# Kernel optimization log

Hardware: AMD Instinct MI355X
Metric: run time of the kernel (lower is better)

The kernel has to match this reference:

```python
import jax, jax.numpy as jnp
import numpy as np

B, L, D, H, DFF, WS = 8, 16384, 256, 8, 1024, 32
HD = D // H
NW = L // WS


def setup_inputs() -> dict:
    key = jax.random.key(0)
    ks = jax.random.split(key, 12)
    p = lambda k, sh: jax.random.normal(k, sh, jnp.float32) * 0.02
    return {
        "query_em": jax.random.normal(ks[0], (B, L, D), jnp.float32),
        "key_value_em": jax.random.normal(ks[1], (B, L, D), jnp.float32),
        "Wq": p(ks[2], (D, D)), "bq": jnp.zeros((D,), jnp.float32),
        "Wk": p(ks[3], (D, D)), "bk": jnp.zeros((D,), jnp.float32),
        "Wv": p(ks[4], (D, D)), "bv": jnp.zeros((D,), jnp.float32),
        "Wo": p(ks[5], (D, D)), "bo": jnp.zeros((D,), jnp.float32),
        "g1": jnp.ones((D,), jnp.float32), "be1": jnp.zeros((D,), jnp.float32),
        "W1": p(ks[6], (D, DFF)), "bf1": jnp.zeros((DFF,), jnp.float32),
        "W2": p(ks[7], (DFF, D)), "bf2": jnp.zeros((D,), jnp.float32),
        "g2": jnp.ones((D,), jnp.float32), "be2": jnp.zeros((D,), jnp.float32),
    }


def _layernorm(x, g, b):
    m = jnp.mean(x, axis=-1, keepdims=True)
    v = jnp.var(x, axis=-1, keepdims=True)
    return (x - m) * jax.lax.rsqrt(v + 1e-5) * g + b


def _encoder_layer(q, kv, Wq, bq, Wk, bk, Wv, bv, Wo, bo, g1, be1, W1, bf1, W2, bf2, g2, be2):
    # q, kv: [B, NW, WS, D] -- attention only within each window of WS tokens
    b, nw, ws, d = q.shape
    qh = (q @ Wq + bq).reshape(b, nw, ws, H, HD)
    kh = (kv @ Wk + bk).reshape(b, nw, ws, H, HD)
    vh = (kv @ Wv + bv).reshape(b, nw, ws, H, HD)
    scores = jnp.einsum("bnqhd,bnkhd->bnhqk", qh, kh) / np.sqrt(HD).astype(np.float32)
    attn = jax.nn.softmax(scores, axis=-1)
    o = jnp.einsum("bnhqk,bnkhd->bnqhd", attn, vh).reshape(b, nw, ws, d)
    o = o @ Wo + bo
    x = _layernorm(q + o, g1, be1)  # post-LN residual
    f = jax.nn.relu(x @ W1 + bf1) @ W2 + bf2
    return _layernorm(x + f, g2, be2)


def reference(query_em, key_value_em, Wq, bq, Wk, bk, Wv, bv, Wo, bo,
              g1, be1, W1, bf1, W2, bf2, g2, be2):
    params = (Wq, bq, Wk, bk, Wv, bv, Wo, bo, g1, be1, W1, bf1, W2, bf2, g2, be2)
    q = query_em.reshape(B, NW, WS, D)
    kv = key_value_em.reshape(B, NW, WS, D)
    x = _encoder_layer(q, kv, *params)
    # cyclic shift by half a window-count along the window axis, second pass, shift back
    x = jnp.roll(x, -WS // 2, axis=1)
    x = _encoder_layer(x, x, *params)
    x = jnp.roll(x, WS // 2, axis=1)
    return x.reshape(B, L, D)
```

## Files before the change

kernel.cpp:

```cpp
#include <hip/hip_runtime.h>
#include <cstdint>
#include <cstddef>

typedef unsigned short u16;
typedef __bf16 bf16x8 __attribute__((ext_vector_type(8)));
typedef float f32x4 __attribute__((ext_vector_type(4)));
typedef unsigned short u16x8 __attribute__((ext_vector_type(8)));
typedef unsigned short u16x4 __attribute__((ext_vector_type(4)));

__device__ __forceinline__ u16 f2bf(float f) {
  union { float f; unsigned u; } x; x.f = f;
  unsigned r = x.u + 0x7fffu + ((x.u >> 16) & 1u);
  return (u16)(r >> 16);
}
__device__ __forceinline__ float bf2f(u16 u) {
  union { unsigned u; float f; } x; x.u = ((unsigned)u) << 16;
  return x.f;
}
__device__ __forceinline__ void gload16(const void* g, void* l) {
  __builtin_amdgcn_global_load_lds(
      (const __attribute__((address_space(1))) unsigned int*)g,
      (__attribute__((address_space(3))) unsigned int*)l, 16, 0, 0);
}

template<int MODE>
__global__ __launch_bounds__(256) void gemm_bt(
    const u16* __restrict__ Ap, int lda, const u16* __restrict__ Bt,
    const float* __restrict__ bias, u16* __restrict__ C0, int ldc, int coff,
    u16* __restrict__ C2, int vsplit, int N, int K, int gy)
{
  __shared__ u16 As[2][128 * 32];
  __shared__ u16 Bs[2][128 * 32];
  const int tid  = threadIdx.x;
  const int lane = tid & 63, w = tid >> 6;
  const int nwg = gridDim.x, o = blockIdx.x;
  const int lid = (o & 7) * (nwg >> 3) + (o >> 3);
  const int by = lid % gy, bx = lid / gy;
  const int row0 = bx * 128, col0 = by * 128;
  const int wr = (w >> 1) * 64, wc = (w & 1) * 64;
  const int fr = lane & 15, fg = lane >> 4;
  const int srow  = (w << 5) + (lane >> 2);
  const int sslot = (lane & 3) ^ ((lane >> 2) & 3);

  auto stage = [&](int buf, int k0) {
    #pragma unroll
    for (int h = 0; h < 2; ++h)
      gload16((const char*)Ap + ((size_t)(row0 + srow + h*16) * lda + k0) * 2 + sslot*16,
              &As[buf][((w << 5) + h*16) * 32]);
    #pragma unroll
    for (int h = 0; h < 2; ++h)
      gload16((const char*)Bt + ((size_t)(col0 + srow + h*16) * K + k0) * 2 + sslot*16,
              &Bs[buf][((w << 5) + h*16) * 32]);
  };

  f32x4 acc[4][4] = {};

  stage(0, 0);
  __syncthreads();
  int cur = 0;
  for (int k0 = 0; k0 < K; k0 += 32) {
    if (k0 + 32 < K) stage(cur ^ 1, k0 + 32);
    bf16x8 af[4], bf[4];
    #pragma unroll
    for (int i = 0; i < 4; ++i) {
      const int r = wr + i*16 + fr;
      af[i] = *(const bf16x8*)&As[cur][r*32 + ((fg ^ (fr & 3)) << 3)];
    }
    #pragma unroll
    for (int j = 0; j < 4; ++j) {
      const int r = wc + j*16 + fr;
      bf[j] = *(const bf16x8*)&Bs[cur][r*32 + ((fg ^ (fr & 3)) << 3)];
    }
    #pragma unroll
    for (int i = 0; i < 4; ++i)
      #pragma unroll
      for (int j = 0; j < 4; ++j)
        acc[i][j] = __builtin_amdgcn_mfma_f32_16x16x32_bf16(af[i], bf[j], acc[i][j], 0, 0, 0);
    __syncthreads();
    cur ^= 1;
  }

  const int vpart = (MODE == 3) || (MODE == 2 && col0 >= vsplit);
  #pragma unroll
  for (int j = 0; j < 4; ++j) {
    const int c  = col0 + wc + j*16 + fr;
    const float bv = bias[c];
    #pragma unroll
    for (int i = 0; i < 4; ++i) {
      if (vpart) {
        const int cv = (MODE == 2) ? c - vsplit : c;
        const int rb = row0 + wr + i*16 + fg*4;
        u16x4 vv;
        #pragma unroll
        for (int t = 0; t < 4; ++t) vv[t] = f2bf(acc[i][j][t] + bv);
        *(u16x4*)&C2[((size_t)(rb >> 5) * 256 + cv) * 32 + (rb & 31)] = vv;
      } else {
        #pragma unroll
        for (int t = 0; t < 4; ++t) {
          const int r = row0 + wr + i*16 + fg*4 + t;
          float v = acc[i][j][t] + bv;
          if (MODE == 1) v = v > 0.f ? v : 0.f;
          C0[(size_t)r * ldc + coff + c] = f2bf(v);
        }
      }
    }
  }
}

template<int OUT_F32>
__global__ __launch_bounds__(512, 2) void ffn_fused(
    const u16* __restrict__ X, const u16* __restrict__ W1T,
    const float* __restrict__ b1, const u16* __restrict__ W2T,
    const float* __restrict__ b2, const float* __restrict__ g,
    const float* __restrict__ be, void* __restrict__ Y)
{
  __shared__ u16 W1s[4][32 * 256];
  __shared__ u16 W2s[4][256 * 32];
  __shared__ u16 Hs[8][32 * 32];
  __shared__ float b1s[1024];
  const int tid = threadIdx.x, lane = tid & 63, w = tid >> 6;
  const int fr = lane & 15, fg = lane >> 4;
  const int row0 = blockIdx.x * 256 + w * 32;
  u16* Hw = &Hs[w][0];
  const int hxor = (fr >> 1) & 3;

  auto stage = [&](int buf, int hb) {
    #pragma unroll
    for (int h = 0; h < 2; ++h) {
      const int r = w*4 + h*2 + (lane >> 5);
      const int sl = (lane & 31) ^ (r & 7);
      gload16((const char*)W1T + ((size_t)((hb << 5) + r) * 256 + sl*8) * 2,
              &W1s[buf][(w*4 + h*2) * 256]);
    }
    #pragma unroll
    for (int h = 0; h < 2; ++h) {
      const int r = w*32 + h*16 + (lane >> 2);
      const int sl = (lane & 3) ^ ((r >> 1) & 3);
      gload16((const char*)W2T + ((size_t)r * 1024 + (hb << 5) + sl*8) * 2,
              &W2s[buf][(w*32 + h*16) * 32]);
    }
  };

  if (tid < 256) {
    f32x4 bv = *(const f32x4*)&b1[tid * 4];
    *(f32x4*)&b1s[tid * 4] = bv;
  }
  bf16x8 af[2][8];
  #pragma unroll
  for (int g2 = 0; g2 < 2; ++g2)
    #pragma unroll
    for (int kf = 0; kf < 8; ++kf)
      af[g2][kf] = *(const bf16x8*)&X[(size_t)(row0 + g2*16 + fr) * 256 + kf*32 + fg*8];
  asm volatile("s_waitcnt vmcnt(0)" ::: "memory");

  f32x4 acc2[2][16] = {};

  auto compute_slice = [&](int hb, int cur) {
    f32x4 acc1[2][2] = {};
    #pragma unroll
    for (int kf = 0; kf < 8; ++kf) {
      #pragma unroll
      for (int hf = 0; hf < 2; ++hf) {
        const int n = hf*16 + fr;
        bf16x8 w1f = *(const bf16x8*)&W1s[cur][n*256 + ((((kf << 2) | fg) ^ (n & 7)) << 3)];
        acc1[hf][0] = __builtin_amdgcn_mfma_f32_16x16x32_bf16(w1f, af[0][kf], acc1[hf][0], 0, 0, 0);
        acc1[hf][1] = __builtin_amdgcn_mfma_f32_16x16x32_bf16(w1f, af[1][kf], acc1[hf][1], 0, 0, 0);
      }
    }
    #pragma unroll
    for (int g2 = 0; g2 < 2; ++g2) {
      #pragma unroll
      for (int hf = 0; hf < 2; ++hf) {
        const int h0 = hf*16 + fg*4;
        f32x4 b4 = *(const f32x4*)&b1s[(hb << 5) + h0];
        u16x4 hv;
        #pragma unroll
        for (int t = 0; t < 4; ++t) {
          float v = acc1[hf][g2][t] + b4[t];
          hv[t] = f2bf(v > 0.f ? v : 0.f);
        }
        const int tok = g2*16 + fr;
        *(u16x4*)((char*)Hw + tok*64 + ((((hf << 1) | (fg >> 1)) ^ hxor) << 4)
                                     + ((fg & 1) << 3)) = hv;
      }
    }
    asm volatile("s_waitcnt lgkmcnt(0)" ::: "memory");
    __builtin_amdgcn_sched_barrier(0);

    bf16x8 hf2[2];
    #pragma unroll
    for (int g2 = 0; g2 < 2; ++g2) {
      const int tok = g2*16 + fr;
      hf2[g2] = *(const bf16x8*)((char*)Hw + tok*64 + ((fg ^ hxor) << 4));
    }
    #pragma unroll
    for (int nf = 0; nf < 16; ++nf) {
      const int n = nf*16 + fr;
      bf16x8 w2f = *(const bf16x8*)&W2s[cur][n*32 + ((fg ^ ((n >> 1) & 3)) << 3)];
      acc2[0][nf] = __builtin_amdgcn_mfma_f32_16x16x32_bf16(hf2[0], w2f, acc2[0][nf], 0, 0, 0);
      acc2[1][nf] = __builtin_amdgcn_mfma_f32_16x16x32_bf16(hf2[1], w2f, acc2[1][nf], 0, 0, 0);
    }
  };

  stage(0, 0);
  stage(1, 1);
  for (int hb = 0; hb < 30; ++hb) {
    stage((hb + 2) & 3, hb + 2);
    asm volatile("s_waitcnt vmcnt(8)" ::: "memory");
    __builtin_amdgcn_s_barrier();
    __builtin_amdgcn_sched_barrier(0);
    compute_slice(hb, hb & 3);
  }
  asm volatile("s_waitcnt vmcnt(4)" ::: "memory");
  __builtin_amdgcn_s_barrier();
  __builtin_amdgcn_sched_barrier(0);
  compute_slice(30, 30 & 3);
  asm volatile("s_waitcnt vmcnt(0)" ::: "memory");
  __builtin_amdgcn_s_barrier();
  __builtin_amdgcn_sched_barrier(0);
  compute_slice(31, 31 & 3);

  #pragma unroll
  for (int g2 = 0; g2 < 2; ++g2) {
    const int rbase = row0 + g2*16 + fg*4;
    float s1[4] = {}, sq[4] = {};
    #pragma unroll
    for (int nf = 0; nf < 16; ++nf) {
      const int c = nf*16 + fr;
      const float b = b2[c];
      #pragma unroll
      for (int t = 0; t < 4; ++t) {
        float v = acc2[g2][nf][t] + b + bf2f(X[(size_t)(rbase + t) * 256 + c]);
        acc2[g2][nf][t] = v;
        s1[t] += v; sq[t] += v * v;
      }
    }
    #pragma unroll
    for (int d = 1; d < 16; d <<= 1) {
      #pragma unroll
      for (int t = 0; t < 4; ++t) {
        s1[t] += __shfl_xor(s1[t], d, 64);
        sq[t] += __shfl_xor(sq[t], d, 64);
      }
    }
    float mean[4], rstd[4];
    #pragma unroll
    for (int t = 0; t < 4; ++t) {
      mean[t] = s1[t] * (1.f/256.f);
      const float var = sq[t] * (1.f/256.f) - mean[t]*mean[t];
      rstd[t] = rsqrtf(var + 1e-5f);
    }
    #pragma unroll
    for (int nf = 0; nf < 16; ++nf) {
      const int c = nf*16 + fr;
      const float gc = g[c], bc = be[c];
      #pragma unroll
      for (int t = 0; t < 4; ++t) {
        const float y = (acc2[g2][nf][t] - mean[t]) * rstd[t] * gc + bc;
        if (OUT_F32) ((float*)Y)[(size_t)(rbase + t) * 256 + c] = y;
        else         ((u16*)Y)[(size_t)(rbase + t) * 256 + c] = f2bf(y);
      }
    }
  }
}

__global__ __launch_bounds__(256) void attn_mfma(
    const u16* Q, int sq, const u16* __restrict__ K, int sk,
    const u16* __restrict__ Vt, u16* O, int so)
{
  __shared__ u16 P[4][32 * 40];
  const int tid = threadIdx.x, lane = tid & 63, w = tid >> 6;
  const int win = blockIdx.x * 4 + w;
  const size_t q0 = (size_t)win * 32;
  const int fr = lane & 15, fg = lane >> 4;
  u16* Pw = &P[w][0];
  const float scale = 0.17677669529663687f;

  for (int h = 0; h < 8; ++h) {
    const int co = h * 32;
    bf16x8 qa[2], kb[2];
    #pragma unroll
    for (int i = 0; i < 2; ++i)
      qa[i] = *(const bf16x8*)&Q[(q0 + i*16 + fr) * sq + co + fg*8];
    #pragma unroll
    for (int j = 0; j < 2; ++j)
      kb[j] = *(const bf16x8*)&K[(q0 + j*16 + fr) * sk + co + fg*8];
    f32x4 s[2][2] = {};
    #pragma unroll
    for (int i = 0; i < 2; ++i)
      #pragma unroll
      for (int j = 0; j < 2; ++j)
        s[i][j] = __builtin_amdgcn_mfma_f32_16x16x32_bf16(qa[i], kb[j], s[i][j], 0, 0, 0);

    float inv[2][4];
    #pragma unroll
    for (int i = 0; i < 2; ++i) {
      #pragma unroll
      for (int t = 0; t < 4; ++t) {
        float a0 = s[i][0][t] * scale, a1 = s[i][1][t] * scale;
        float mx = fmaxf(a0, a1);
        #pragma unroll
        for (int d = 1; d < 16; d <<= 1) mx = fmaxf(mx, __shfl_xor(mx, d, 64));
        const float p0 = __expf(a0 - mx), p1 = __expf(a1 - mx);
        float sm = p0 + p1;
        #pragma unroll
        for (int d = 1; d < 16; d <<= 1) sm += __shfl_xor(sm, d, 64);
        inv[i][t] = 1.f / sm;
        const int q = i*16 + fg*4 + t;
        Pw[q*40 + fr]      = f2bf(p0);
        Pw[q*40 + 16 + fr] = f2bf(p1);
      }
    }

    bf16x8 pa[2], vb[2];
    #pragma unroll
    for (int i = 0; i < 2; ++i)
      pa[i] = *(const bf16x8*)&Pw[(i*16 + fr)*40 + fg*8];
    #pragma unroll
    for (int j = 0; j < 2; ++j)
      vb[j] = *(const bf16x8*)&Vt[(size_t)win*8192 + (co + j*16 + fr)*32 + fg*8];
    f32x4 oacc[2][2] = {};
    #pragma unroll
    for (int i = 0; i < 2; ++i)
      #pragma unroll
      for (int j = 0; j < 2; ++j)
        oacc[i][j] = __builtin_amdgcn_mfma_f32_16x16x32_bf16(pa[i], vb[j], oacc[i][j], 0, 0, 0);

    #pragma unroll
    for (int i = 0; i < 2; ++i)
      #pragma unroll
      for (int j = 0; j < 2; ++j)
        #pragma unroll
        for (int t = 0; t < 4; ++t)
          O[(q0 + i*16 + fg*4 + t) * so + co + j*16 + fr] =
              f2bf(oacc[i][j][t] * inv[i][t]);
  }
}

__global__ __launch_bounds__(256) void ln_resid(
    const u16* __restrict__ X, const u16* __restrict__ R,
    const float* __restrict__ g, const float* __restrict__ be,
    u16* __restrict__ Y)
{
  const int tid = threadIdx.x;
  const int lane = tid & 63, w = tid >> 6;
  const size_t row = (size_t)blockIdx.x * 4 + w;
  const size_t off = row * 256 + (size_t)(lane << 2);
  u16x4 xb = *(const u16x4*)&X[off];
  u16x4 rb = *(const u16x4*)&R[off];
  const float v0 = bf2f(xb[0]) + bf2f(rb[0]), v1 = bf2f(xb[1]) + bf2f(rb[1]);
  const float v2 = bf2f(xb[2]) + bf2f(rb[2]), v3 = bf2f(xb[3]) + bf2f(rb[3]);
  float s  = v0 + v1 + v2 + v3;
  float s2 = v0*v0 + v1*v1 + v2*v2 + v3*v3;
  #pragma unroll
  for (int d = 1; d < 64; d <<= 1) {
    s  += __shfl_xor(s,  d, 64);
    s2 += __shfl_xor(s2, d, 64);
  }
  const float m   = s  * (1.f/256.f);
  const float var = s2 * (1.f/256.f) - m*m;
  const float rs  = rsqrtf(var + 1e-5f);
  f32x4 gg = *(const f32x4*)&g[lane << 2];
  f32x4 bb = *(const f32x4*)&be[lane << 2];
  u16x4 oo = { f2bf((v0 - m) * rs * gg[0] + bb[0]),
               f2bf((v1 - m) * rs * gg[1] + bb[1]),
               f2bf((v2 - m) * rs * gg[2] + bb[2]),
               f2bf((v3 - m) * rs * gg[3] + bb[3]) };
  *(u16x4*)&Y[off] = oo;
}

__global__ __launch_bounds__(256) void wprep(
    const float* __restrict__ W, u16* __restrict__ Wt, int K, int N)
{
  const int idx = blockIdx.x * 256 + threadIdx.x;
  if (idx >= K * N) return;
  const int k = idx / N, n = idx - k * N;
  Wt[(size_t)n * K + k] = f2bf(W[idx]);
}

__global__ __launch_bounds__(256) void bcat(
    const float* __restrict__ a, const float* __restrict__ b,
    const float* __restrict__ c, float* __restrict__ o)
{
  const int i = blockIdx.x * 256 + threadIdx.x;
  o[i] = i < 256 ? a[i] : (i < 512 ? b[i - 256] : c[i - 512]);
}

__global__ __launch_bounds__(256) void f32_to_bf16(
    const float* __restrict__ X, u16* __restrict__ Y)
{
  const size_t i = ((size_t)blockIdx.x * 256 + threadIdx.x) * 8;
  f32x4 a = *(const f32x4*)&X[i];
  f32x4 b = *(const f32x4*)&X[i + 4];
  u16x8 o = { f2bf(a[0]), f2bf(a[1]), f2bf(a[2]), f2bf(a[3]),
              f2bf(b[0]), f2bf(b[1]), f2bf(b[2]), f2bf(b[3]) };
  *(u16x8*)&Y[i] = o;
}

extern "C" void kernel_launch(void* const* d_in, const int* in_sizes, int n_in,
                              void* d_out, int out_size, void* d_ws, size_t ws_size,
                              hipStream_t stream)
{
  const float* query  = (const float*)d_in[0];
  const float* keyval = (const float*)d_in[1];
  const float* Wq = (const float*)d_in[2];  const float* bq  = (const float*)d_in[3];
  const float* Wk = (const float*)d_in[4];  const float* bk  = (const float*)d_in[5];
  const float* Wv = (const float*)d_in[6];  const float* bv  = (const float*)d_in[7];
  const float* Wo = (const float*)d_in[8];  const float* bo  = (const float*)d_in[9];
  const float* g1 = (const float*)d_in[10]; const float* be1 = (const float*)d_in[11];
  const float* W1 = (const float*)d_in[12]; const float* bf1 = (const float*)d_in[13];
  const float* W2 = (const float*)d_in[14]; const float* bf2 = (const float*)d_in[15];
  const float* g2 = (const float*)d_in[16]; const float* be2 = (const float*)d_in[17];

  const int M = 131072;
  char* ws = (char*)d_ws;
  u16*  xcur = (u16*)ws;
  u16*  x1   = (u16*)(ws + (64ull  << 20));
  u16*  kvb  = (u16*)(ws + (128ull << 20));
  u16*  tmp  = (u16*)(ws + (192ull << 20));
  u16*  QKc  = (u16*)(ws + (256ull << 20));
  u16*  Vtc  = (u16*)(ws + (384ull << 20));
  u16*  WqkvT = (u16*)(ws + (448ull << 20));
  u16*  WoT   = WqkvT + 196608;
  u16*  W1T   = WoT   + 65536;
  u16*  W2T   = W1T   + 262144;
  float* bqkv = (float*)(W2T + 262144);
  float* bkv  = bqkv + 256;

  wprep<<<256,  256, 0, stream>>>(Wq, WqkvT,          256, 256);
  wprep<<<256,  256, 0, stream>>>(Wk, WqkvT +  65536, 256, 256);
  wprep<<<256,  256, 0, stream>>>(Wv, WqkvT + 131072, 256, 256);
  wprep<<<256,  256, 0, stream>>>(Wo, WoT, 256, 256);
  wprep<<<1024, 256, 0, stream>>>(W1, W1T, 256, 1024);
  wprep<<<1024, 256, 0, stream>>>(W2, W2T, 1024, 256);
  bcat<<<3, 256, 0, stream>>>(bq, bk, bv, bqkv);
  f32_to_bf16<<<16384, 256, 0, stream>>>(query,  xcur);
  f32_to_bf16<<<16384, 256, 0, stream>>>(keyval, kvb);

  auto run_layer = [&](int first, int last) {
    if (first) {
      gemm_bt<0><<<2048, 256, 0, stream>>>(
          xcur, 256, WqkvT, bq, QKc, 512, 0, nullptr, 0, 256, 256, 2);
      gemm_bt<2><<<4096, 256, 0, stream>>>(
          kvb, 256, WqkvT + 65536, bkv, QKc, 512, 256, Vtc, 256, 512, 256, 4);
    } else {
      gemm_bt<2><<<6144, 256, 0, stream>>>(
          xcur, 256, WqkvT, bqkv, QKc, 512, 0, Vtc, 512, 768, 256, 6);
    }
    attn_mfma<<<1024, 256, 0, stream>>>(QKc, 512, QKc + 256, 512, Vtc, QKc, 512);
    gemm_bt<0><<<2048, 256, 0, stream>>>(
        QKc, 512, WoT, bo, tmp, 256, 0, nullptr, 0, 256, 256, 2);
    ln_resid<<<M/4, 256, 0, stream>>>(tmp, xcur, g1, be1, x1);
    if (last) ffn_fused<1><<<512, 512, 0, stream>>>(
        x1, W1T, bf1, W2T, bf2, g2, be2, d_out);
    else      ffn_fused<0><<<512, 512, 0, stream>>>(
        x1, W1T, bf1, W2T, bf2, g2, be2, xcur);
  };

  run_layer(1, 0);
  run_layer(0, 1);
}
```

Baseline: 938.1 us.

## Fuse output projection GEMM with residual add and LayerNorm

Replaces the separate Wo GEMM and ln_resid kernels with one kernel. Each block computes full 128x256 output rows, adds bias and residual, reduces row statistics through shuffles and shared memory, and writes the normalized bf16 result. This removes the round trip of the intermediate tensor through global memory and one kernel launch per layer. In exchange it uses a new tiling with 512 threads and more LDS, and its epilogue does scalar strided residual loads and stores.

```diff
diff --git a/kernel.cpp b/kernel.cpp
--- a/kernel.cpp
+++ b/kernel.cpp
@@ -107,6 +107,122 @@
   }
 }
 
+__global__ __launch_bounds__(512) void gemm_oln(
+    const u16* __restrict__ Ap, int lda, const u16* __restrict__ Bt,
+    const float* __restrict__ bias, const u16* __restrict__ Res,
+    const float* __restrict__ g, const float* __restrict__ be,
+    u16* __restrict__ Y, int K)
+{
+  __shared__ u16 As[2][128 * 32];
+  __shared__ u16 Bs[2][256 * 32];
+  __shared__ float2 red[128][4];
+  __shared__ float2 stats[128];
+  const int tid  = threadIdx.x;
+  const int lane = tid & 63, w = tid >> 6;
+  const int nwg = gridDim.x, o = blockIdx.x;
+  const int lid = (o & 7) * (nwg >> 3) + (o >> 3);
+  const int row0 = lid * 128;
+  const int wr = (w >> 2) * 64, wc = (w & 3) * 64;
+  const int fr = lane & 15, fg = lane >> 4;
+  const int sr   = lane >> 2;
+  const int sslot = (lane & 3) ^ ((lane >> 2) & 3);
+
+  auto stage = [&](int buf, int k0) {
+    gload16((const char*)Ap + ((size_t)(row0 + (w << 4) + sr) * lda + k0) * 2 + sslot*16,
+            &As[buf][((w << 4)) * 32]);
+    #pragma unroll
+    for (int h = 0; h < 2; ++h)
+      gload16((const char*)Bt + ((size_t)((w << 5) + h*16 + sr) * K + k0) * 2 + sslot*16,
+              &Bs[buf][((w << 5) + h*16) * 32]);
+  };
+
+  f32x4 acc[4][4] = {};
+
+  stage(0, 0);
+  __syncthreads();
+  int cur = 0;
+  for (int k0 = 0; k0 < K; k0 += 32) {
+    if (k0 + 32 < K) stage(cur ^ 1, k0 + 32);
+    bf16x8 af[4], bf[4];
+    #pragma unroll
+    for (int i = 0; i < 4; ++i) {
+      const int r = wr + i*16 + fr;
+      af[i] = *(const bf16x8*)&As[cur][r*32 + ((fg ^ (fr & 3)) << 3)];
+    }
+    #pragma unroll
+    for (int j = 0; j < 4; ++j) {
+      const int r = wc + j*16 + fr;
+      bf[j] = *(const bf16x8*)&Bs[cur][r*32 + ((fg ^ (fr & 3)) << 3)];
+    }
+    #pragma unroll
+    for (int i = 0; i < 4; ++i)
+      #pragma unroll
+      for (int j = 0; j < 4; ++j)
+        acc[i][j] = __builtin_amdgcn_mfma_f32_16x16x32_bf16(af[i], bf[j], acc[i][j], 0, 0, 0);
+    __syncthreads();
+    cur ^= 1;
+  }
+
+  float ps[4][4] = {}, pq[4][4] = {};
+  #pragma unroll
+  for (int j = 0; j < 4; ++j) {
+    const int c = wc + j*16 + fr;
+    const float bv = bias[c];
+    #pragma unroll
+    for (int i = 0; i < 4; ++i) {
+      #pragma unroll
+      for (int t = 0; t < 4; ++t) {
+        const int r = row0 + wr + i*16 + fg*4 + t;
+        float v = acc[i][j][t] + bv + bf2f(Res[(size_t)r * 256 + c]);
+        acc[i][j][t] = v;
+        ps[i][t] += v;
+        pq[i][t] += v * v;
+      }
+    }
+  }
+  #pragma unroll
+  for (int d = 1; d < 16; d <<= 1) {
+    #pragma unroll
+    for (int i = 0; i < 4; ++i)
+      #pragma unroll
+      for (int t = 0; t < 4; ++t) {
+        ps[i][t] += __shfl_xor(ps[i][t], d, 64);
+        pq[i][t] += __shfl_xor(pq[i][t], d, 64);
+      }
+  }
+  if (fr == 0) {
+    #pragma unroll
+    for (int i = 0; i < 4; ++i)
+      #pragma unroll
+      for (int t = 0; t < 4; ++t)
+        red[wr + i*16 + fg*4 + t][w & 3] = make_float2(ps[i][t], pq[i][t]);
+  }
+  __syncthreads();
+  if (tid < 128) {
+    float S = 0.f, Q = 0.f;
+    #pragma unroll
+    for (int ww = 0; ww < 4; ++ww) { float2 p = red[tid][ww]; S += p.x; Q += p.y; }
+    const float m = S * (1.f/256.f);
+    const float var = Q * (1.f/256.f) - m*m;
+    stats[tid] = make_float2(m, rsqrtf(var + 1e-5f));
+  }
+  __syncthreads();
+  #pragma unroll
+  for (int i = 0; i < 4; ++i) {
+    #pragma unroll
+    for (int t = 0; t < 4; ++t) {
+      const int rl = wr + i*16 + fg*4 + t;
+      const float2 st = stats[rl];
+      const size_t r = row0 + rl;
+      #pragma unroll
+      for (int j = 0; j < 4; ++j) {
+        const int c = wc + j*16 + fr;
+        Y[r * 256 + c] = f2bf((acc[i][j][t] - st.x) * st.y * g[c] + be[c]);
+      }
+    }
+  }
+}
+
 template<int OUT_F32>
 __global__ __launch_bounds__(512, 2) void ffn_fused(
     const u16* __restrict__ X, const u16* __restrict__ W1T,
@@ -337,38 +453,6 @@
   }
 }
 
-__global__ __launch_bounds__(256) void ln_resid(
-    const u16* __restrict__ X, const u16* __restrict__ R,
-    const float* __restrict__ g, const float* __restrict__ be,
-    u16* __restrict__ Y)
-{
-  const int tid = threadIdx.x;
-  const int lane = tid & 63, w = tid >> 6;
-  const size_t row = (size_t)blockIdx.x * 4 + w;
-  const size_t off = row * 256 + (size_t)(lane << 2);
-  u16x4 xb = *(const u16x4*)&X[off];
-  u16x4 rb = *(const u16x4*)&R[off];
-  const float v0 = bf2f(xb[0]) + bf2f(rb[0]), v1 = bf2f(xb[1]) + bf2f(rb[1]);
-  const float v2 = bf2f(xb[2]) + bf2f(rb[2]), v3 = bf2f(xb[3]) + bf2f(rb[3]);
-  float s  = v0 + v1 + v2 + v3;
-  float s2 = v0*v0 + v1*v1 + v2*v2 + v3*v3;
-  #pragma unroll
-  for (int d = 1; d < 64; d <<= 1) {
-    s  += __shfl_xor(s,  d, 64);
-    s2 += __shfl_xor(s2, d, 64);
-  }
-  const float m   = s  * (1.f/256.f);
-  const float var = s2 * (1.f/256.f) - m*m;
-  const float rs  = rsqrtf(var + 1e-5f);
-  f32x4 gg = *(const f32x4*)&g[lane << 2];
-  f32x4 bb = *(const f32x4*)&be[lane << 2];
-  u16x4 oo = { f2bf((v0 - m) * rs * gg[0] + bb[0]),
-               f2bf((v1 - m) * rs * gg[1] + bb[1]),
-               f2bf((v2 - m) * rs * gg[2] + bb[2]),
-               f2bf((v3 - m) * rs * gg[3] + bb[3]) };
-  *(u16x4*)&Y[off] = oo;
-}
-
 __global__ __launch_bounds__(256) void wprep(
     const float* __restrict__ W, u16* __restrict__ Wt, int K, int N)
 {
@@ -417,7 +501,6 @@
   u16*  xcur = (u16*)ws;
   u16*  x1   = (u16*)(ws + (64ull  << 20));
   u16*  kvb  = (u16*)(ws + (128ull << 20));
-  u16*  tmp  = (u16*)(ws + (192ull << 20));
   u16*  QKc  = (u16*)(ws + (256ull << 20));
   u16*  Vtc  = (u16*)(ws + (384ull << 20));
   u16*  WqkvT = (u16*)(ws + (448ull << 20));
@@ -448,9 +531,8 @@
           xcur, 256, WqkvT, bqkv, QKc, 512, 0, Vtc, 512, 768, 256, 6);
     }
     attn_mfma<<<1024, 256, 0, stream>>>(QKc, 512, QKc + 256, 512, Vtc, QKc, 512);
-    gemm_bt<0><<<2048, 256, 0, stream>>>(
-        QKc, 512, WoT, bo, tmp, 256, 0, nullptr, 0, 256, 256, 2);
-    ln_resid<<<M/4, 256, 0, stream>>>(tmp, xcur, g1, be1, x1);
+    gemm_oln<<<1024, 512, 0, stream>>>(
+        QKc, 512, WoT, bo, xcur, g1, be1, x1, 256);
     if (last) ffn_fused<1><<<512, 512, 0, stream>>>(
         x1, W1T, bf1, W2T, bf2, g2, be2, d_out);
     else      ffn_fused<0><<<512, 512, 0, stream>>>(
```

Result: faster. 909.8 us (-3.0%).
